# Optimization experiments

Measured on AMD Instinct MI355X. Metric: run time of the kernel, lower is better.

The kernel has to match this reference:

```python
import jax, jax.numpy as jnp
import numpy as np

N_NODES = 100000
N_EDGES = 3200000
D = 32


def _gat(x, edge_index, W, att_s, att_d, bias, heads, ch, neg_slope):
    """PyG-style GATConv (shared lin for src/dst, add_self_loops=False).
    x: [N, D_in], edge_index: [2, E], W: [heads*ch, D_in],
    att_s/att_d: [heads, ch], bias: [heads*ch]. Returns [N, heads*ch]."""
    n = x.shape[0]
    h = (x @ W.T).reshape(n, heads, ch)                      # [N,H,C]
    a_s = (h * att_s[None]).sum(-1)                           # [N,H]
    a_d = (h * att_d[None]).sum(-1)                           # [N,H]
    src, dst = edge_index[0], edge_index[1]
    logits = jax.nn.leaky_relu(a_s[src] + a_d[dst], neg_slope)  # [E,H]
    # segment softmax over edges grouped by destination node
    m = jax.ops.segment_max(logits, dst, num_segments=n)     # [N,H]
    m = jnp.where(jnp.isfinite(m), m, 0.0)                    # nodes w/ no in-edges
    ex = jnp.exp(logits - m[dst])                             # [E,H]
    denom = jax.ops.segment_sum(ex, dst, num_segments=n)     # [N,H]
    alpha = ex / (denom[dst] + 1e-16)                         # [E,H]
    out = jax.ops.segment_sum(alpha[:, :, None] * h[src], dst, num_segments=n)  # [N,H,C]
    return out.reshape(n, heads * ch) + bias


def setup_inputs() -> dict:
    key = jax.random.key(0)
    ks = jax.random.split(key, 16)
    x = jax.random.normal(ks[0], (N_NODES, D), dtype=jnp.float32)
    edge_index = jax.random.randint(ks[1], (2, N_EDGES), 0, N_NODES, dtype=jnp.int64)
    s = 1.0 / np.sqrt(D)
    return {
        "x": x,
        "edge_index": edge_index,
        "W1": jax.random.normal(ks[2], (32, D), dtype=jnp.float32) * s,
        "att_s1": jax.random.normal(ks[3], (2, 16), dtype=jnp.float32) * 0.05,
        "att_d1": jax.random.normal(ks[4], (2, 16), dtype=jnp.float32) * 0.05,
        "b1": jnp.full((32,), 0.1, dtype=jnp.float32),
        "ea1": jnp.ones((1,), dtype=jnp.float32),  # edge_activator
        "W2": jax.random.normal(ks[5], (32, 32), dtype=jnp.float32) * s,
        "att_s2": jax.random.normal(ks[6], (2, 16), dtype=jnp.float32) * 0.05,
        "att_d2": jax.random.normal(ks[7], (2, 16), dtype=jnp.float32) * 0.05,
        "b2": jnp.full((32,), 0.1, dtype=jnp.float32),
        "W3": jax.random.normal(ks[8], (32, 32), dtype=jnp.float32) * s,
        "att_s3": jax.random.normal(ks[9], (1, 32), dtype=jnp.float32) * 0.05,
        "att_d3": jax.random.normal(ks[10], (1, 32), dtype=jnp.float32) * 0.05,
        "b3": jnp.full((32,), 0.1, dtype=jnp.float32),
    }


def reference(x, edge_index, W1, att_s1, att_d1, b1, ea1,
              W2, att_s2, att_d2, b2, W3, att_s3, att_d3, b3):
    # --- layer 1 (negative_slope=0.01) ---
    h = _gat(x, edge_index, W1, att_s1, att_d1, b1, heads=2, ch=16, neg_slope=0.01)
    scale = jnp.tanh(ea1)[0]
    scale = jnp.where(scale < 0.1, 1.0, scale)  # 'continue' branch skips the scaling
    h = h * scale
    h = h + 0.05 * jax.lax.stop_gradient(h)      # h + 0.05*h.detach()
    h = jax.nn.elu(h)                            # eval path (training=False)
    h = jnp.clip(h, -3.0, 3.0)
    # --- layer 2 (default negative_slope=0.2) ---
    h = _gat(h, edge_index, W2, att_s2, att_d2, b2, heads=2, ch=16, neg_slope=0.2)
    h = jax.nn.elu(h)
    h = jnp.clip(h, -3.0, 3.0)
    # --- layer 3: heads=1, concat=False ---
    out = _gat(h, edge_index, W3, att_s3, att_d3, b3, heads=1, ch=32, neg_slope=0.2)
    return out
```

## Files before the change

kernel.cpp:

```cpp
#include <hip/hip_runtime.h>
#include <hip/hip_bf16.h>
#include <hip/hip_fp16.h>


#define NPB  128
#define CAPB 6144
#define PAD_SENTINEL 0xFFFFFFFFu

__global__ void k_initcur(int* __restrict__ cursor, int nb) {
    int i = blockIdx.x * 256 + threadIdx.x;
    if (i < nb) cursor[i] = i * CAPB;
}

__global__ void __launch_bounds__(1024)
k_bin(const int* __restrict__ src, const int* __restrict__ dst,
      int* __restrict__ bucket_cursor, unsigned int* __restrict__ pairs,
      int e, int nb) {
    const int EPT = 8;
    __shared__ int h[1024];
    __shared__ int cbase[1024];
    __shared__ int room[1024];
    int t = threadIdx.x;
    for (int i = t; i < nb; i += 1024) h[i] = 0;
    __syncthreads();
    int e4 = e >> 2;
    int base4 = blockIdx.x * 2048;
    int boff[EPT];
    unsigned int pk[EPT];
#pragma unroll
    for (int k = 0; k < 2; k++) {
        int i4 = base4 + k * 1024 + t;
        if (i4 < e4) {
            int4 dv = ((const int4*)dst)[i4];
            int4 sv = ((const int4*)src)[i4];
            const int* dd = (const int*)&dv;
            const int* ss = (const int*)&sv;
#pragma unroll
            for (int j = 0; j < 4; j++) {
                int q = 4 * k + j;
                int d = dd[j];
                int b = d >> 7;
                pk[q] = ((unsigned int)ss[j] << 7) | (unsigned int)(d & 127);
                int off = atomicAdd(&h[b], 1);
                boff[q] = (b << 16) | off;
            }
        } else {
#pragma unroll
            for (int j = 0; j < 4; j++) boff[4 * k + j] = -1;
        }
    }
    __syncthreads();
    for (int i = t; i < nb; i += 1024) {
        int c = h[i];
        if (c) {
            int r = (c + 7) & ~7;
            int cb = atomicAdd(&bucket_cursor[i], r);
            int rm = (i + 1) * CAPB - cb;
            cbase[i] = cb;
            room[i] = rm;
            for (int j = c; j < r && j < rm; j++)
                pairs[cb + j] = PAD_SENTINEL;
        }
    }
    __syncthreads();
#pragma unroll
    for (int q = 0; q < EPT; q++) {
        if (boff[q] >= 0) {
            int b = boff[q] >> 16;
            int off = boff[q] & 0xFFFF;
            if (off < room[b]) pairs[cbase[b] + off] = pk[q];
        }
    }
    if (blockIdx.x == 0 && t < (e & 3)) {
        int i = (e & ~3) + t;
        int d = dst[i];
        int b = d >> 7;
        int pos = atomicAdd(&bucket_cursor[b], 1);
        if (pos < (b + 1) * CAPB)
            pairs[pos] = ((unsigned int)src[i] << 7) | (unsigned int)(d & 127);
    }
}

__global__ void __launch_bounds__(512)
k_bucket_sort(const unsigned int* __restrict__ pairs,
              const int* __restrict__ bucket_cursor,
              int2* __restrict__ rowinfo, int* __restrict__ src_sorted,
              int n) {
    __shared__ int cnt[NPB];
    __shared__ int cur[NPB];
    __shared__ int total;
    __shared__ unsigned int lp[CAPB];
    __shared__ int op[CAPB];
    int b = blockIdx.x;
    int t = threadIdx.x;
    int bbase = b * CAPB;
    int m = bucket_cursor[b] - bbase;
    if (m > CAPB) m = CAPB;
    if (t < NPB) cnt[t] = 0;
    __syncthreads();
    for (int cb = 0; cb < m; cb += 4096) {
        unsigned int pv[8];
#pragma unroll
        for (int u = 0; u < 8; u++) {
            int i = cb + u * 512 + t;
            pv[u] = (i < m) ? pairs[bbase + i] : PAD_SENTINEL;
        }
#pragma unroll
        for (int u = 0; u < 8; u++) {
            int i = cb + u * 512 + t;
            if (i < m) lp[i] = pv[u];
            if (pv[u] != PAD_SENTINEL) atomicAdd(&cnt[pv[u] & 127], 1);
        }
    }
    __syncthreads();
    if (t < 64) {
        int c0 = cnt[2 * t];
        int c1 = cnt[2 * t + 1];
        int sum = c0 + c1;
        int run = sum;
#pragma unroll
        for (int off = 1; off < 64; off <<= 1) {
            int v = __shfl_up(run, off, 64);
            if (t >= off) run += v;
        }
        int ex = run - sum;
        cur[2 * t] = ex;
        cur[2 * t + 1] = ex + c0;
        int node = b * NPB + 2 * t;
        if (node < n) rowinfo[node] = make_int2(bbase + ex, c0);
        if (node + 1 < n) rowinfo[node + 1] = make_int2(bbase + ex + c0, c1);
        if (t == 63) total = run;
    }
    __syncthreads();
    for (int cb = 0; cb < m; cb += 4096) {
        unsigned int pv[8];
        int of[8];
#pragma unroll
        for (int u = 0; u < 8; u++) {
            int i = cb + u * 512 + t;
            pv[u] = (i < m) ? lp[i] : PAD_SENTINEL;
        }
#pragma unroll
        for (int u = 0; u < 8; u++)
            if (pv[u] != PAD_SENTINEL) of[u] = atomicAdd(&cur[pv[u] & 127], 1);
#pragma unroll
        for (int u = 0; u < 8; u++)
            if (pv[u] != PAD_SENTINEL) op[of[u]] = (int)(pv[u] >> 7);
    }
    __syncthreads();
    int nt4 = (total + 3) >> 2;
    int4* dst4 = (int4*)(src_sorted + bbase);
    const int4* src4 = (const int4*)op;
    for (int i = t; i < nt4; i += 512) dst4[i] = src4[i];
}

template <int H>
__global__ void k_transform(const float* __restrict__ in, const float* __restrict__ W,
                            const float* __restrict__ att_s, const float* __restrict__ att_d,
                            __half* __restrict__ h16, float* __restrict__ a_s,
                            float* __restrict__ a_d, int n) {
    constexpr int C = 32 / H;
    __shared__ float Wl[32][33];
    __shared__ float xs[8][32];
    int t = threadIdx.x;
    for (int i = t; i < 1024; i += 256) Wl[i >> 5][i & 31] = W[i];
    int nl = t >> 5, o = t & 31;
    int node = blockIdx.x * 8 + nl;
    xs[nl][o] = (node < n) ? in[node * 32 + o] : 0.f;
    __syncthreads();
    float acc = 0.f;
#pragma unroll
    for (int k = 0; k < 32; k++) acc = fmaf(xs[nl][k], Wl[o][k], acc);
    if (node < n) {
        h16[node * 32 + o] = __float2half_rn(acc);
        float vs = acc * att_s[o];
        float vd = acc * att_d[o];
#pragma unroll
        for (int m = C / 2; m >= 1; m >>= 1) {
            vs += __shfl_xor(vs, m, 64);
            vd += __shfl_xor(vd, m, 64);
        }
        if ((o % C) == 0) {
            int hh = o / C;
            a_s[node * H + hh] = vs;
            a_d[node * H + hh] = vd;
        }
    }
}

template <int H, int EPI>
__global__ void k_edge(const int2* __restrict__ rowinfo, const int* __restrict__ src_sorted,
                       const __half* __restrict__ h16,
                       const float* __restrict__ a_s, const float* __restrict__ a_d,
                       const float* __restrict__ bias, const float* __restrict__ ea,
                       float* __restrict__ out, int n, float slope) {
    constexpr int CAP = 160;
    constexpr int RSTR = 2 * CAP + 16;
    __shared__ int lds_raw[4][H][RSTR];
    int wid = threadIdx.x >> 6;
    int lane = threadIdx.x & 63;
    int node = blockIdx.x * 4 + wid;
    if (node >= n) return;
    int2 bi = rowinfo[node];
    int beg = bi.x, deg = bi.y;
    int padded = (deg + 31) & ~31;

    float ad[H];
#pragma unroll
    for (int hh = 0; hh < H; hh++) ad[hh] = a_d[node * H + hh];

    float ds[H];
#pragma unroll
    for (int hh = 0; hh < H; hh++) ds[hh] = 0.f;
    bool fast = (padded <= CAP);
    if (fast) {
        for (int idx = lane; idx < padded; idx += 64) {
            if (idx < deg) {
                int s = src_sorted[beg + idx];
                if (H == 2) {
                    float2 as2 = *(const float2*)((const char*)a_s + (unsigned)(s << 3));
                    float l0 = as2.x + ad[0]; l0 = fmaxf(l0, l0 * slope);
                    float l1 = as2.y + ad[1]; l1 = fmaxf(l1, l1 * slope);
                    float e0 = __expf(l0), e1 = __expf(l1);
                    ds[0] += e0; ds[1] += e1;
                    ((int2*)lds_raw[wid][0])[idx] = make_int2(s, __float_as_int(e0));
                    ((int2*)lds_raw[wid][H - 1])[idx] = make_int2(s, __float_as_int(e1));
                } else {
                    float l0 = a_s[s] + ad[0]; l0 = fmaxf(l0, l0 * slope);
                    float e0 = __expf(l0);
                    ds[0] += e0;
                    ((int2*)lds_raw[wid][0])[idx] = make_int2(s, __float_as_int(e0));
                }
            } else {
#pragma unroll
                for (int hh = 0; hh < H; hh++)
                    ((int2*)lds_raw[wid][hh])[idx] = make_int2(0, 0);
            }
        }
    } else {
        for (int idx = lane; idx < deg; idx += 64) {
            int s = src_sorted[beg + idx];
            if (H == 2) {
                float2 as2 = *(const float2*)((const char*)a_s + (unsigned)(s << 3));
                float l0 = as2.x + ad[0]; l0 = fmaxf(l0, l0 * slope);
                float l1 = as2.y + ad[1]; l1 = fmaxf(l1, l1 * slope);
                ds[0] += __expf(l0); ds[1] += __expf(l1);
            } else {
                float l0 = a_s[s] + ad[0]; l0 = fmaxf(l0, l0 * slope);
                ds[0] += __expf(l0);
            }
        }
    }

    int e4 = lane >> 4;
    int l16 = lane & 15;
    int hd = (H == 2) ? (l16 >> 3) : 0;
    int co = l16 << 2;
    float adh = ad[hd];
    float acc0 = 0.f, acc1 = 0.f;
    const char* hbase = (const char*)h16;
    const int* lb = &lds_raw[wid][hd][e4 * 4];

    if (fast) {
        for (int base = 0; base < padded; base += 32) {
            int4 qa = *(const int4*)(lb + base * 2);
            int4 qb = *(const int4*)(lb + base * 2 + 16);
            int4 qc = *(const int4*)(lb + base * 2 + 32);
            int4 qd = *(const int4*)(lb + base * 2 + 48);
            __half2 h0 = *(const __half2*)(hbase + (unsigned)((qa.x << 6) + co));
            __half2 h1 = *(const __half2*)(hbase + (unsigned)((qa.z << 6) + co));
            __half2 h2 = *(const __half2*)(hbase + (unsigned)((qb.x << 6) + co));
            __half2 h3 = *(const __half2*)(hbase + (unsigned)((qb.z << 6) + co));
            __half2 h4 = *(const __half2*)(hbase + (unsigned)((qc.x << 6) + co));
            __half2 h5 = *(const __half2*)(hbase + (unsigned)((qc.z << 6) + co));
            __half2 h6 = *(const __half2*)(hbase + (unsigned)((qd.x << 6) + co));
            __half2 h7 = *(const __half2*)(hbase + (unsigned)((qd.z << 6) + co));
            float xa0 = __int_as_float(qa.y), xa1 = __int_as_float(qa.w);
            float xb0 = __int_as_float(qb.y), xb1 = __int_as_float(qb.w);
            float xc0 = __int_as_float(qc.y), xc1 = __int_as_float(qc.w);
            float xd0 = __int_as_float(qd.y), xd1 = __int_as_float(qd.w);
            acc0 = fmaf(xa0, __half2float(__low2half(h0)), acc0);
            acc1 = fmaf(xa0, __half2float(__high2half(h0)), acc1);
            acc0 = fmaf(xa1, __half2float(__low2half(h1)), acc0);
            acc1 = fmaf(xa1, __half2float(__high2half(h1)), acc1);
            acc0 = fmaf(xb0, __half2float(__low2half(h2)), acc0);
            acc1 = fmaf(xb0, __half2float(__high2half(h2)), acc1);
            acc0 = fmaf(xb1, __half2float(__low2half(h3)), acc0);
            acc1 = fmaf(xb1, __half2float(__high2half(h3)), acc1);
            acc0 = fmaf(xc0, __half2float(__low2half(h4)), acc0);
            acc1 = fmaf(xc0, __half2float(__high2half(h4)), acc1);
            acc0 = fmaf(xc1, __half2float(__low2half(h5)), acc0);
            acc1 = fmaf(xc1, __half2float(__high2half(h5)), acc1);
            acc0 = fmaf(xd0, __half2float(__low2half(h6)), acc0);
            acc1 = fmaf(xd0, __half2float(__high2half(h6)), acc1);
            acc0 = fmaf(xd1, __half2float(__low2half(h7)), acc0);
            acc1 = fmaf(xd1, __half2float(__high2half(h7)), acc1);
        }
    } else {
        for (int base = 0; base < deg; base += 16) {
#pragma unroll
            for (int u = 0; u < 4; u++) {
                int idx = base + u * 4 + e4;
                int s = 0;
                float ex = 0.f;
                if (idx < deg) {
                    s = src_sorted[beg + idx];
                    float l = a_s[s * H + hd] + adh;
                    l = fmaxf(l, l * slope);
                    ex = __expf(l);
                }
                __half2 hv = *(const __half2*)(hbase + (unsigned)((s << 6) + co));
                acc0 = fmaf(ex, __half2float(__low2half(hv)), acc0);
                acc1 = fmaf(ex, __half2float(__high2half(hv)), acc1);
            }
        }
    }

#pragma unroll
    for (int hh = 0; hh < H; hh++) {
        float v = ds[hh];
#pragma unroll
        for (int m = 32; m >= 1; m >>= 1) v += __shfl_xor(v, m, 64);
        ds[hh] = 1.f / (v + 1e-16f);
    }

#pragma unroll
    for (int m = 16; m <= 32; m <<= 1) {
        acc0 += __shfl_xor(acc0, m, 64);
        acc1 += __shfl_xor(acc1, m, 64);
    }

    if (lane < 16) {
        float invd = ds[hd];
        float2 bv = *(const float2*)(bias + l16 * 2);
        float v0 = fmaf(acc0, invd, bv.x);
        float v1 = fmaf(acc1, invd, bv.y);
        if (EPI == 1) {
            float s0 = tanhf(ea[0]);
            if (s0 < 0.1f) s0 = 1.0f;
            s0 *= 1.05f;
            v0 *= s0; v1 *= s0;
            v0 = (v0 > 0.f) ? v0 : expm1f(v0);
            v1 = (v1 > 0.f) ? v1 : expm1f(v1);
            v0 = fminf(3.f, fmaxf(-3.f, v0));
            v1 = fminf(3.f, fmaxf(-3.f, v1));
        } else if (EPI == 2) {
            v0 = (v0 > 0.f) ? v0 : expm1f(v0);
            v1 = (v1 > 0.f) ? v1 : expm1f(v1);
            v0 = fminf(3.f, fmaxf(-3.f, v0));
            v1 = fminf(3.f, fmaxf(-3.f, v1));
        }
        *(float2*)(out + (size_t)node * 32 + l16 * 2) = make_float2(v0, v1);
    }
}

extern "C" void kernel_launch(void* const* d_in, const int* in_sizes, int n_in,
                              void* d_out, int out_size, void* d_ws, size_t ws_size,
                              hipStream_t stream) {
    const float* x   = (const float*)d_in[0];
    const int*   ei  = (const int*)d_in[1];
    const float* W1  = (const float*)d_in[2];
    const float* as1 = (const float*)d_in[3];
    const float* ad1 = (const float*)d_in[4];
    const float* b1  = (const float*)d_in[5];
    const float* ea1 = (const float*)d_in[6];
    const float* W2  = (const float*)d_in[7];
    const float* as2 = (const float*)d_in[8];
    const float* ad2 = (const float*)d_in[9];
    const float* b2  = (const float*)d_in[10];
    const float* W3  = (const float*)d_in[11];
    const float* as3 = (const float*)d_in[12];
    const float* ad3 = (const float*)d_in[13];
    const float* b3  = (const float*)d_in[14];
    float* out = (float*)d_out;

    const int n = in_sizes[0] / 32;
    const int e = in_sizes[1] / 2;
    const int* src = ei;
    const int* dst = ei + e;
    const int nb = (n + NPB - 1) / NPB;

    char* w = (char*)d_ws;
    auto alloc = [&](size_t bytes) -> void* {
        void* p = (void*)w;
        w += (bytes + 255) & ~(size_t)255;
        return p;
    };
    __half* h16     = (__half*)alloc((size_t)n * 32 * 2);
    float* a_s      = (float*)alloc((size_t)n * 2 * 4);
    float* a_d      = (float*)alloc((size_t)n * 2 * 4);
    float* bufA     = (float*)alloc((size_t)n * 32 * 4);
    float* bufB     = (float*)alloc((size_t)n * 32 * 4);
    int2* rowinfo   = (int2*)alloc((size_t)n * 8);
    int* bucket_cur = (int*)alloc((size_t)(nb + 1) * 4);
    int* src_sorted = (int*)alloc((size_t)nb * CAPB * 4);
    unsigned int* pairs = (unsigned int*)bufA;

    k_initcur<<<(nb + 255) / 256, 256, 0, stream>>>(bucket_cur, nb);
    int e4 = e >> 2;
    k_bin<<<(e4 + 2047) / 2048, 1024, 0, stream>>>(src, dst, bucket_cur, pairs, e, nb);
    k_bucket_sort<<<nb, 512, 0, stream>>>(pairs, bucket_cur, rowinfo, src_sorted, n);

    const int tgrid = (n + 7) / 8;
    const int egrid = (n + 3) / 4;

    k_transform<2><<<tgrid, 256, 0, stream>>>(x, W1, as1, ad1, h16, a_s, a_d, n);
    k_edge<2, 1><<<egrid, 256, 0, stream>>>(rowinfo, src_sorted, h16, a_s, a_d, b1, ea1, bufA, n, 0.01f);

    k_transform<2><<<tgrid, 256, 0, stream>>>(bufA, W2, as2, ad2, h16, a_s, a_d, n);
    k_edge<2, 2><<<egrid, 256, 0, stream>>>(rowinfo, src_sorted, h16, a_s, a_d, b2, nullptr, bufB, n, 0.2f);

    k_transform<1><<<tgrid, 256, 0, stream>>>(bufB, W3, as3, ad3, h16, a_s, a_d, n);
    k_edge<1, 0><<<egrid, 256, 0, stream>>>(rowinfo, src_sorted, h16, a_s, a_d, b3, nullptr, out, n, 0.2f);
}
```

Measured before the change: 356.6 us.

## Assign one destination node per half-wavefront in GAT edge kernel

The edge aggregation kernel now maps each destination node to 32 lanes instead of a full 64-lane wavefront, so each 256-thread block handles 8 nodes. Padding drops from multiples of 32 to multiples of 16, and the LDS fast-path capacity shrinks to 128 edges per node. This targets lanes left idle on low-degree nodes (average degree about 32) and wasted padded iterations. In exchange, each lane handles more edges serially, and two nodes sharing one wavefront diverge when their degrees differ.

```diff
diff --git a/kernel.cpp b/kernel.cpp
--- a/kernel.cpp
+++ b/kernel.cpp
@@ -194,16 +194,16 @@
                        const float* __restrict__ a_s, const float* __restrict__ a_d,
                        const float* __restrict__ bias, const float* __restrict__ ea,
                        float* __restrict__ out, int n, float slope) {
-    constexpr int CAP = 160;
+    constexpr int CAP = 128;
     constexpr int RSTR = 2 * CAP + 16;
-    __shared__ int lds_raw[4][H][RSTR];
-    int wid = threadIdx.x >> 6;
-    int lane = threadIdx.x & 63;
-    int node = blockIdx.x * 4 + wid;
+    __shared__ int lds_raw[8][H][RSTR];
+    int nw = threadIdx.x >> 5;
+    int hl = threadIdx.x & 31;
+    int node = blockIdx.x * 8 + nw;
     if (node >= n) return;
     int2 bi = rowinfo[node];
     int beg = bi.x, deg = bi.y;
-    int padded = (deg + 31) & ~31;
+    int padB = (deg + 15) & ~15;
 
     float ad[H];
 #pragma unroll
@@ -212,9 +212,9 @@
     float ds[H];
 #pragma unroll
     for (int hh = 0; hh < H; hh++) ds[hh] = 0.f;
-    bool fast = (padded <= CAP);
+    bool fast = (padB <= CAP);
     if (fast) {
-        for (int idx = lane; idx < padded; idx += 64) {
+        for (int idx = hl; idx < padB; idx += 32) {
             if (idx < deg) {
                 int s = src_sorted[beg + idx];
                 if (H == 2) {
@@ -223,22 +223,22 @@
                     float l1 = as2.y + ad[1]; l1 = fmaxf(l1, l1 * slope);
                     float e0 = __expf(l0), e1 = __expf(l1);
                     ds[0] += e0; ds[1] += e1;
-                    ((int2*)lds_raw[wid][0])[idx] = make_int2(s, __float_as_int(e0));
-                    ((int2*)lds_raw[wid][H - 1])[idx] = make_int2(s, __float_as_int(e1));
+                    ((int2*)lds_raw[nw][0])[idx] = make_int2(s, __float_as_int(e0));
+                    ((int2*)lds_raw[nw][H - 1])[idx] = make_int2(s, __float_as_int(e1));
                 } else {
                     float l0 = a_s[s] + ad[0]; l0 = fmaxf(l0, l0 * slope);
                     float e0 = __expf(l0);
                     ds[0] += e0;
-                    ((int2*)lds_raw[wid][0])[idx] = make_int2(s, __float_as_int(e0));
+                    ((int2*)lds_raw[nw][0])[idx] = make_int2(s, __float_as_int(e0));
                 }
             } else {
 #pragma unroll
                 for (int hh = 0; hh < H; hh++)
-                    ((int2*)lds_raw[wid][hh])[idx] = make_int2(0, 0);
+                    ((int2*)lds_raw[nw][hh])[idx] = make_int2(0, 0);
             }
         }
     } else {
-        for (int idx = lane; idx < deg; idx += 64) {
+        for (int idx = hl; idx < deg; idx += 32) {
             int s = src_sorted[beg + idx];
             if (H == 2) {
                 float2 as2 = *(const float2*)((const char*)a_s + (unsigned)(s << 3));
@@ -252,21 +252,21 @@
         }
     }
 
-    int e4 = lane >> 4;
-    int l16 = lane & 15;
+    int e2 = hl >> 4;
+    int l16 = hl & 15;
     int hd = (H == 2) ? (l16 >> 3) : 0;
     int co = l16 << 2;
     float adh = ad[hd];
     float acc0 = 0.f, acc1 = 0.f;
     const char* hbase = (const char*)h16;
-    const int* lb = &lds_raw[wid][hd][e4 * 4];
+    const int* lb = &lds_raw[nw][hd][e2 * 4];
 
     if (fast) {
-        for (int base = 0; base < padded; base += 32) {
+        for (int base = 0; base < padB; base += 16) {
             int4 qa = *(const int4*)(lb + base * 2);
-            int4 qb = *(const int4*)(lb + base * 2 + 16);
-            int4 qc = *(const int4*)(lb + base * 2 + 32);
-            int4 qd = *(const int4*)(lb + base * 2 + 48);
+            int4 qb = *(const int4*)(lb + base * 2 + 8);
+            int4 qc = *(const int4*)(lb + base * 2 + 16);
+            int4 qd = *(const int4*)(lb + base * 2 + 24);
             __half2 h0 = *(const __half2*)(hbase + (unsigned)((qa.x << 6) + co));
             __half2 h1 = *(const __half2*)(hbase + (unsigned)((qa.z << 6) + co));
             __half2 h2 = *(const __half2*)(hbase + (unsigned)((qb.x << 6) + co));
@@ -299,8 +299,8 @@
     } else {
         for (int base = 0; base < deg; base += 16) {
 #pragma unroll
-            for (int u = 0; u < 4; u++) {
-                int idx = base + u * 4 + e4;
+            for (int u = 0; u < 8; u++) {
+                int idx = base + u * 2 + e2;
                 int s = 0;
                 float ex = 0.f;
                 if (idx < deg) {
@@ -320,17 +320,14 @@
     for (int hh = 0; hh < H; hh++) {
         float v = ds[hh];
 #pragma unroll
-        for (int m = 32; m >= 1; m >>= 1) v += __shfl_xor(v, m, 64);
+        for (int m = 16; m >= 1; m >>= 1) v += __shfl_xor(v, m, 64);
         ds[hh] = 1.f / (v + 1e-16f);
     }
 
-#pragma unroll
-    for (int m = 16; m <= 32; m <<= 1) {
-        acc0 += __shfl_xor(acc0, m, 64);
-        acc1 += __shfl_xor(acc1, m, 64);
-    }
-
-    if (lane < 16) {
+    acc0 += __shfl_xor(acc0, 16, 64);
+    acc1 += __shfl_xor(acc1, 16, 64);
+
+    if (l16 == hl) {
         float invd = ds[hd];
         float2 bv = *(const float2*)(bias + l16 * 2);
         float v0 = fmaf(acc0, invd, bv.x);
@@ -402,7 +399,7 @@
     k_bucket_sort<<<nb, 512, 0, stream>>>(pairs, bucket_cur, rowinfo, src_sorted, n);
 
     const int tgrid = (n + 7) / 8;
-    const int egrid = (n + 3) / 4;
+    const int egrid = (n + 7) / 8;
 
     k_transform<2><<<tgrid, 256, 0, stream>>>(x, W1, as1, ad1, h16, a_s, a_d, n);
     k_edge<2, 1><<<egrid, 256, 0, stream>>>(rowinfo, src_sorted, h16, a_s, a_d, b1, ea1, bufA, n, 0.01f);
```

Measured after the change: 338.7 us. 1.05x faster.
